# Optimization experiments

Hardware: AMD Instinct MI355X
Metric: run time of the kernel (lower is better)

## Reference

```python
import jax, jax.numpy as jnp
import numpy as np

B, N, E, R = 2, 4096, 1024, 128   # batch, seq_len, embed_dim, expand_ratio (head_dim)
H = E // R                        # num heads (scalar decay per head)
EPS = 1e-5                        # torch LayerNorm default eps


def _silu(x):
    return x * jax.nn.sigmoid(x)


def setup_inputs() -> dict:
    key = jax.random.key(0)
    ks = jax.random.split(key, 12)
    std = 0.02

    def w(k, shape):
        return jax.random.normal(k, shape, jnp.float32) * std

    return {
        "x": jax.random.normal(ks[0], (B, N, E), jnp.float32),
        # log of lower bound of the decay gate; must be negative so exp() in (0,1)
        "log_lower_bound": -jax.random.uniform(ks[1], (H,), jnp.float32, minval=0.1, maxval=3.0),
        "Wq": w(ks[2], (E, E)),
        "Wk": w(ks[3], (E, E)),
        "Wv": w(ks[4], (E, E)),
        "Wf": w(ks[5], (H, E)),      # f_proj: embed_dim -> embed_dim // expand_ratio
        "Wb1": w(ks[6], (R, E)),     # bet_proj low-rank
        "Wb2": w(ks[7], (E, R)),
        "Wg1": w(ks[8], (R, E)),     # output_gate low-rank
        "Wg2": w(ks[9], (E, R)),
        "gamma": jnp.ones((E,), jnp.float32),  # LayerNorm weight (bias=False)
        "Wo": w(ks[10], (E, E)),
    }


def _simple_gla(q, k, v, g):
    """Gated linear attention recurrence (fla simple_gla semantics).
    q,k,v: [B,H,N,R]; g: [B,H,N] (log decay per head per step).
    S_t = exp(g_t) * S_{t-1} + k_t v_t^T ;  o_t = (q_t * d^-0.5) @ S_t
    """
    scale = q.shape[-1] ** -0.5
    qT = jnp.moveaxis(q, 2, 0)  # [N,B,H,R]
    kT = jnp.moveaxis(k, 2, 0)
    vT = jnp.moveaxis(v, 2, 0)
    gT = jnp.moveaxis(g, 2, 0)  # [N,B,H]

    S0 = jnp.zeros((q.shape[0], q.shape[1], q.shape[-1], v.shape[-1]), q.dtype)

    def step(S, inp):
        qt, kt, vt, gt = inp
        S = S * jnp.exp(gt)[..., None, None] + kt[..., :, None] * vt[..., None, :]
        o = jnp.einsum('bhk,bhkv->bhv', qt * scale, S)
        return S, o

    _, o = jax.lax.scan(step, S0, (qT, kT, vT, gT))
    return jnp.moveaxis(o, 0, 2)  # [B,H,N,R]


def reference(x, log_lower_bound, Wq, Wk, Wv, Wf, Wb1, Wb2, Wg1, Wg2, gamma, Wo):
    # projections + activations
    q = _silu(x @ Wq.T)
    k = _silu(x @ Wk.T)
    v = x @ Wv.T
    f = x @ Wf.T                      # [B,N,H] scalar decay logits per head

    # householder q-transform with dense-memory beta (normalized reflection vector)
    beta = _silu((x @ Wb1.T) @ Wb2.T)  # [B,N,E]
    bn = beta * jax.lax.rsqrt(jnp.sum(beta * beta, -1, keepdims=True) + 1e-12)
    q = q - 2.0 * jnp.sum(q * bn, -1, keepdims=True) * bn

    def split_heads(t):  # [B,N,E] -> [B,H,N,R]
        return jnp.moveaxis(t.reshape(B, N, H, R), 2, 1)

    qh, kh, vh = split_heads(q), split_heads(k), split_heads(v)

    # log-space decay gate with lower bound
    lb = jnp.exp(log_lower_bound)                      # [H] in (0,1)
    fg = lb + (1.0 - lb) * jax.nn.sigmoid(f)           # [B,N,H]
    log_f = jnp.transpose(jnp.log(fg), (0, 2, 1))      # [B,H,N]

    o = _simple_gla(qh, kh, vh, log_f)                 # [B,H,N,R]
    o = jnp.moveaxis(o, 1, 2).reshape(B, N, E)

    # output gate
    gate = jax.nn.sigmoid((x @ Wg1.T) @ Wg2.T)
    o = o * gate

    # LayerNorm (weight only, bias=False)
    mu = jnp.mean(o, -1, keepdims=True)
    var = jnp.mean((o - mu) ** 2, -1, keepdims=True)
    o = (o - mu) * jax.lax.rsqrt(var + EPS) * gamma

    return o @ Wo.T
```

## Files before the change

kernel.cpp:

```cpp
#include <hip/hip_runtime.h>
#include <hip/hip_bf16.h>

using u16 = unsigned short;
typedef __attribute__((ext_vector_type(8))) short bf16x8;
typedef __attribute__((ext_vector_type(4))) float f32x4;
typedef __attribute__((ext_vector_type(8))) u16 u16x8;
typedef __attribute__((ext_vector_type(4))) u16 u16x4;

#define B_ 2
#define N_ 4096
#define E_ 1024
#define R_ 128
#define H_ 8
#define M_ 8192
#define CHUNK_ 128
#define NC_ 32
#define BH_ 16

__device__ __forceinline__ float b2f(u16 u) { return __uint_as_float(((unsigned)u) << 16); }
__device__ __forceinline__ u16 f2b(float f) {
  unsigned u = __float_as_uint(f);
  return (u16)((u + 0x7fffu + ((u >> 16) & 1u)) >> 16);
}
__device__ __forceinline__ float sigm(float x) {
  return __builtin_amdgcn_rcpf(1.0f + __expf(-x));
}

#define GLDS(g, l) __builtin_amdgcn_global_load_lds( \
    (const __attribute__((address_space(1))) unsigned int*)(g), \
    (__attribute__((address_space(3))) unsigned int*)(l), 16, 0, 0)

struct CvtArgs {
  const float* src[10];
  u16* dst[11];
};

__global__ void __launch_bounds__(256) cvt_all(CvtArgs a) {
  int idx = blockIdx.x * 256 + threadIdx.x;
  const int SZ[11] = {2097152, 262144, 262144, 262144, 2048,
                      32768, 32768, 32768, 32768, 262144, 30720};
  int off = idx, seg = 0;
#pragma unroll
  for (int i = 0; i < 10; i++) {
    if (seg == i && off >= SZ[i]) { off -= SZ[i]; seg = i + 1; }
  }
  u16x4 z = (u16x4){0, 0, 0, 0};
  if (seg == 10) { ((u16x4*)a.dst[10])[off] = z; return; }
  float4 v = ((const float4*)a.src[seg])[off];
  u16x4 r;
  r[0] = f2b(v.x); r[1] = f2b(v.y); r[2] = f2b(v.z); r[3] = f2b(v.w);
  if (seg == 6) {
    int n = off >> 5, c = off & 31;
    u16x4* W2 = (u16x4*)a.dst[6];
    W2[n * 64 + c] = r; W2[n * 64 + 32 + c] = z;
  } else if (seg == 8) {
    int n = off >> 5, c = off & 31;
    u16x4* W2 = (u16x4*)a.dst[8];
    W2[(1024 + n) * 64 + 32 + c] = r; W2[(1024 + n) * 64 + c] = z;
  } else {
    ((u16x4*)a.dst[seg])[off] = r;
  }
}

template<bool SWAP>
__device__ __forceinline__ void mfma_panel(f32x4 (&acc)[4][4], const u16* A, const u16* Bm,
                                           int wr, int wc, int l15, int q8) {
  bf16x8 af[4], bf[4];
#pragma unroll
  for (int mi = 0; mi < 4; mi++) af[mi] = *(const bf16x8*)&A[(wr * 64 + mi * 16 + l15) * 32 + q8];
#pragma unroll
  for (int ni = 0; ni < 4; ni++) bf[ni] = *(const bf16x8*)&Bm[(wc * 64 + ni * 16 + l15) * 32 + q8];
#pragma unroll
  for (int mi = 0; mi < 4; mi++)
#pragma unroll
    for (int ni = 0; ni < 4; ni++)
      acc[mi][ni] = SWAP
        ? __builtin_amdgcn_mfma_f32_16x16x32_bf16(bf[ni], af[mi], acc[mi][ni], 0, 0, 0)
        : __builtin_amdgcn_mfma_f32_16x16x32_bf16(af[mi], bf[ni], acc[mi][ni], 0, 0, 0);
}

template<bool SWAP, int K>
__device__ __forceinline__ void gemm_loop(const u16* __restrict__ X, const u16* __restrict__ W,
                                          int m0, int n0,
                                          u16* As, u16* Bs, f32x4 (&acc)[4][4], int tid) {
  const int wave = tid >> 6, lane = tid & 63;
  const int wr = wave >> 1, wc = wave & 1, l15 = lane & 15, q8 = (lane >> 4) * 8;
  const u16* Ap = X + (size_t)(m0 + wave * 32 + (lane >> 2)) * K + (lane & 3) * 8;
  const u16* Bp = W + (size_t)(n0 + wave * 32 + (lane >> 2)) * K + (lane & 3) * 8;
  u16* A0 = As + wave * 1024;
  u16* B0 = Bs + wave * 1024;
#pragma unroll
  for (int k0 = 0; k0 < K; k0 += 64) {
    GLDS(Ap + k0,                    A0);
    GLDS(Ap + 16 * (size_t)K + k0,   A0 + 512);
    GLDS(Ap + k0 + 32,               A0 + 4096);
    GLDS(Ap + 16 * (size_t)K + k0 + 32, A0 + 4608);
    GLDS(Bp + k0,                    B0);
    GLDS(Bp + 16 * (size_t)K + k0,   B0 + 512);
    GLDS(Bp + k0 + 32,               B0 + 4096);
    GLDS(Bp + 16 * (size_t)K + k0 + 32, B0 + 4608);
    __syncthreads();
    mfma_panel<SWAP>(acc, As, Bs, wr, wc, l15, q8);
    mfma_panel<SWAP>(acc, As + 4096, Bs + 4096, wr, wc, l15, q8);
    __syncthreads();
  }
}

__global__ void __launch_bounds__(256) mega_gemm(const u16* __restrict__ X, const u16* __restrict__ Wcat,
                                                 const float* __restrict__ llb,
                                                 u16* __restrict__ Qb, u16* __restrict__ Kb,
                                                 u16* __restrict__ KT, u16* __restrict__ VT,
                                                 u16* __restrict__ T1, float* __restrict__ LOGF) {
  __shared__ u16 sh[17408];
  u16* As = sh;
  u16* Bs = sh + 8192;
  u16* Ts = sh;
  const int tid = threadIdx.x;
  const int m0 = blockIdx.y * 128;
  const int ny = blockIdx.x, n0 = ny * 128;
  const int wave = tid >> 6, lane = tid & 63;
  const int wr = wave >> 1, wc = wave & 1, l15 = lane & 15, q4 = (lane >> 4) * 4;
  f32x4 acc[4][4];
#pragma unroll
  for (int i = 0; i < 4; i++)
#pragma unroll
    for (int j = 0; j < 4; j++) acc[i][j] = (f32x4){0.f, 0.f, 0.f, 0.f};

  if (ny >= 16 && ny < 24) {
    gemm_loop<false, 1024>(X, Wcat, m0, n0, As, Bs, acc, tid);
#pragma unroll
    for (int mi = 0; mi < 4; mi++) {
#pragma unroll
      for (int ni = 0; ni < 4; ni++) {
        int col = n0 - 2048 + wc * 64 + ni * 16 + l15;
        int rbase = m0 + wr * 64 + mi * 16 + q4;
        int head = col >> 7, rl = col & 127;
        int bb = rbase >> 12, nseq = rbase & (N_ - 1);
        u16x4 pk;
#pragma unroll
        for (int r = 0; r < 4; r++) pk[r] = f2b(acc[mi][ni][r]);
        *(u16x4*)&VT[((size_t)(bb * H_ + head) * R_ + rl) * N_ + nseq] = pk;
      }
    }
    return;
  }

  gemm_loop<true, 1024>(X, Wcat, m0, n0, As, Bs, acc, tid);

  if (ny == 26) {
    if (wc == 0 && (lane >> 4) < 2) {
#pragma unroll
      for (int mi = 0; mi < 4; mi++) {
        int mcol = m0 + wr * 64 + mi * 16 + l15;
        int bb = mcol >> 12, nseq = mcol & (N_ - 1);
#pragma unroll
        for (int r = 0; r < 4; r++) {
          int h = q4 + r;
          float lb = __expf(llb[h]);
          LOGF[(size_t)(bb * H_ + h) * N_ + nseq] =
              __logf(lb + (1.f - lb) * sigm(acc[mi][0][r]));
        }
      }
    }
    return;
  }

#pragma unroll
  for (int mi = 0; mi < 4; mi++) {
#pragma unroll
    for (int ni = 0; ni < 4; ni++) {
      int nb = n0 + wc * 64 + ni * 16 + q4;
      int mcol = m0 + wr * 64 + mi * 16 + l15;
      u16x4 pk;
#pragma unroll
      for (int r = 0; r < 4; r++) {
        float v = acc[mi][ni][r];
        if (ny < 16) v = v * sigm(v);
        pk[r] = f2b(v);
      }
      if (ny < 8) {
        *(u16x4*)&Qb[(size_t)mcol * E_ + nb] = pk;
      } else if (ny < 16) {
        *(u16x4*)&Kb[(size_t)mcol * E_ + nb - 1024] = pk;
        int nl = nb - n0;
        int ml = mcol - m0;
#pragma unroll
        for (int r = 0; r < 4; r++) Ts[(nl + r) * 136 + ml] = pk[r];
      } else {
        *(u16x4*)&T1[(size_t)mcol * 256 + nb - 3072] = pk;
      }
    }
  }

  if (ny >= 8 && ny < 16) {
    __syncthreads();
    int head = (n0 - 1024) >> 7;
    int bb = m0 >> 12, nloc = m0 & (N_ - 1);
    size_t base = ((size_t)(bb * H_ + head) * R_) * N_ + nloc;
#pragma unroll
    for (int p = 0; p < 8; p++) {
      int nl = p * 16 + (tid >> 4);
      int m8 = (tid & 15) * 8;
      u16x8 v = *(const u16x8*)&Ts[nl * 136 + m8];
      *(u16x8*)&KT[base + (size_t)nl * N_ + m8] = v;
    }
  }
}

__global__ void __launch_bounds__(256) bg_gemm(const u16* __restrict__ T1, const u16* __restrict__ W2,
                                               u16* __restrict__ BETA, u16* __restrict__ GATE) {
  __shared__ u16 As[8192];
  __shared__ u16 Bs[8192];
  const int tid = threadIdx.x;
  const int m0 = blockIdx.x * 128;
  const int n0 = blockIdx.y * 128;
  f32x4 acc[4][4];
#pragma unroll
  for (int i = 0; i < 4; i++)
#pragma unroll
    for (int j = 0; j < 4; j++) acc[i][j] = (f32x4){0.f, 0.f, 0.f, 0.f};
  gemm_loop<true, 256>(T1, W2, m0, n0, As, Bs, acc, tid);
  const int wave = tid >> 6, lane = tid & 63;
  const int wr = wave >> 1, wc = wave & 1, l15 = lane & 15, q4 = (lane >> 4) * 4;
#pragma unroll
  for (int mi = 0; mi < 4; mi++) {
#pragma unroll
    for (int ni = 0; ni < 4; ni++) {
      int nb = n0 + wc * 64 + ni * 16 + q4;
      int mcol = m0 + wr * 64 + mi * 16 + l15;
      u16x4 pk;
      if (nb < 1024) {
#pragma unroll
        for (int r = 0; r < 4; r++) {
          float v = acc[mi][ni][r];
          pk[r] = f2b(v * sigm(v));
        }
        *(u16x4*)&BETA[(size_t)mcol * E_ + nb] = pk;
      } else {
#pragma unroll
        for (int r = 0; r < 4; r++) pk[r] = f2b(sigm(acc[mi][ni][r]));
        *(u16x4*)&GATE[(size_t)mcol * E_ + nb - 1024] = pk;
      }
    }
  }
}

__global__ void __launch_bounds__(256) out_gemm(const u16* __restrict__ X, const u16* __restrict__ W,
                                                float* __restrict__ C) {
  __shared__ u16 As[8192];
  __shared__ u16 Bs[8192];
  const int tid = threadIdx.x;
  const int m0 = blockIdx.x * 128;
  const int n0 = blockIdx.y * 128;
  f32x4 acc[4][4];
#pragma unroll
  for (int i = 0; i < 4; i++)
#pragma unroll
    for (int j = 0; j < 4; j++) acc[i][j] = (f32x4){0.f, 0.f, 0.f, 0.f};
  gemm_loop<true, 1024>(X, W, m0, n0, As, Bs, acc, tid);
  const int wave = tid >> 6, lane = tid & 63;
  const int wr = wave >> 1, wc = wave & 1, l15 = lane & 15, q4 = (lane >> 4) * 4;
#pragma unroll
  for (int mi = 0; mi < 4; mi++) {
#pragma unroll
    for (int ni = 0; ni < 4; ni++) {
      int nb = n0 + wc * 64 + ni * 16 + q4;
      int mcol = m0 + wr * 64 + mi * 16 + l15;
      *(f32x4*)&C[(size_t)mcol * E_ + nb] = acc[mi][ni];
    }
  }
}

__global__ void __launch_bounds__(256) householder(u16* __restrict__ Q, const u16* __restrict__ BETA) {
  int row = blockIdx.x;
  int tid = threadIdx.x;
  u16* q = Q + (size_t)row * E_;
  const u16* bt = BETA + (size_t)row * E_;
  u16x4 q4 = *(const u16x4*)(q + tid * 4);
  u16x4 b4 = *(const u16x4*)(bt + tid * 4);
  float qv[4], bv[4];
#pragma unroll
  for (int i = 0; i < 4; i++) { qv[i] = b2f(q4[i]); bv[i] = b2f(b4[i]); }
  float ss = bv[0]*bv[0] + bv[1]*bv[1] + bv[2]*bv[2] + bv[3]*bv[3];
  float qd = qv[0]*bv[0] + qv[1]*bv[1] + qv[2]*bv[2] + qv[3]*bv[3];
  __shared__ float red[8];
#pragma unroll
  for (int m = 1; m < 64; m <<= 1) { ss += __shfl_xor(ss, m); qd += __shfl_xor(qd, m); }
  int wid = tid >> 6;
  if ((tid & 63) == 0) { red[wid] = ss; red[4 + wid] = qd; }
  __syncthreads();
  ss = red[0] + red[1] + red[2] + red[3];
  qd = red[4] + red[5] + red[6] + red[7];
  float coef = 2.f * qd / (ss + 1e-12f);
  const float scale = 0.08838834764831845f;
  u16x4 o4;
#pragma unroll
  for (int i = 0; i < 4; i++) o4[i] = f2b((qv[i] - coef * bv[i]) * scale);
  *(u16x4*)(q + tid * 4) = o4;
}

__device__ __forceinline__ void scan_chunk(const float* __restrict__ lf, float* cum, int tid) {
  if (tid < 64) {
    float a = lf[tid], b = lf[tid + 64];
#pragma unroll
    for (int off = 1; off < 64; off <<= 1) {
      float t = __shfl_up(a, off);  if (tid >= off) a += t;
      float t2 = __shfl_up(b, off); if (tid >= off) b += t2;
    }
    b += __shfl(a, 63);
    cum[tid] = a; cum[tid + 64] = b;
  }
  __syncthreads();
}

__device__ __forceinline__ void stage32(u16* dst, const u16* src, size_t stride, int tid) {
  int r0 = tid >> 2, c8 = (tid & 3) * 8;
  *(u16x8*)&dst[(size_t)r0 * 40 + c8] = *(const u16x8*)&src[(size_t)r0 * stride + c8];
  int r1 = r0 + 64;
  *(u16x8*)&dst[(size_t)r1 * 40 + c8] = *(const u16x8*)&src[(size_t)r1 * stride + c8];
}

__device__ __forceinline__ void stage32_scaled(u16* dst, const u16* src, size_t stride,
                                               const float* w, int j0, int tid) {
  int c8 = (tid & 3) * 8;
  float wv[8];
#pragma unroll
  for (int i = 0; i < 8; i++) wv[i] = w[j0 + c8 + i];
#pragma unroll
  for (int rr = 0; rr < 128; rr += 64) {
    int r = rr + (tid >> 2);
    u16x8 raw = *(const u16x8*)&src[(size_t)r * stride + c8];
    u16x8 o;
#pragma unroll
    for (int i = 0; i < 8; i++) o[i] = f2b(b2f(raw[i]) * wv[i]);
    *(u16x8*)&dst[(size_t)r * 40 + c8] = o;
  }
}

template<bool SWAP>
__device__ __forceinline__ void mfma16(f32x4 (&acc)[4][4], const u16* A, const u16* Bm,
                                       int wr, int wc, int l15, int q8) {
  bf16x8 af[4], bf[4];
#pragma unroll
  for (int mi = 0; mi < 4; mi++) af[mi] = *(const bf16x8*)&A[(wr * 64 + mi * 16 + l15) * 40 + q8];
#pragma unroll
  for (int ni = 0; ni < 4; ni++) bf[ni] = *(const bf16x8*)&Bm[(wc * 64 + ni * 16 + l15) * 40 + q8];
#pragma unroll
  for (int mi = 0; mi < 4; mi++)
#pragma unroll
    for (int ni = 0; ni < 4; ni++)
      acc[mi][ni] = SWAP
        ? __builtin_amdgcn_mfma_f32_16x16x32_bf16(bf[ni], af[mi], acc[mi][ni], 0, 0, 0)
        : __builtin_amdgcn_mfma_f32_16x16x32_bf16(af[mi], bf[ni], acc[mi][ni], 0, 0, 0);
}

__global__ void __launch_bounds__(256) gla_phaseA(const u16* __restrict__ KT, const u16* __restrict__ VT,
                                                  const float* __restrict__ LOGF,
                                                  u16* __restrict__ U, float* __restrict__ DC) {
  const int blk = blockIdx.x;
  const int bh = blk >> 5, c = blk & 31;
  const int tid = threadIdx.x;
  const int wave = tid >> 6, lane = tid & 63;
  const int wr = wave >> 1, wc = wave & 1, l15 = lane & 15, q8 = (lane >> 4) * 8;
  __shared__ u16 SA[128 * 40];
  __shared__ u16 SB[128 * 40];
  __shared__ float cum[CHUNK_];
  __shared__ float wd[CHUNK_];
  scan_chunk(LOGF + (size_t)bh * N_ + c * CHUNK_, cum, tid);
  if (tid < 128) wd[tid] = __expf(cum[127] - cum[tid]);
  __syncthreads();
  const u16* vbase = VT + ((size_t)bh * R_) * N_ + (size_t)c * CHUNK_;
  const u16* kbase = KT + ((size_t)bh * R_) * N_ + (size_t)c * CHUNK_;
  f32x4 acc[4][4];
#pragma unroll
  for (int i = 0; i < 4; i++)
#pragma unroll
    for (int j = 0; j < 4; j++) acc[i][j] = (f32x4){0.f, 0.f, 0.f, 0.f};
  for (int j0 = 0; j0 < CHUNK_; j0 += 32) {
    __syncthreads();
    stage32(SA, vbase + j0, N_, tid);
    stage32_scaled(SB, kbase + j0, N_, wd, j0, tid);
    __syncthreads();
    mfma16<true>(acc, SA, SB, wr, wc, l15, q8);
  }
  u16* Up = U + (size_t)blk * (R_ * R_);
  const int q4 = (lane >> 4) * 4;
#pragma unroll
  for (int mi = 0; mi < 4; mi++) {
#pragma unroll
    for (int ni = 0; ni < 4; ni++) {
      int v = wr * 64 + mi * 16 + l15;
      int kb = wc * 64 + ni * 16 + q4;
      u16x4 pk;
#pragma unroll
      for (int r = 0; r < 4; r++) pk[r] = f2b(acc[mi][ni][r]);
      *(u16x4*)&Up[(size_t)v * R_ + kb] = pk;
    }
  }
  if (tid == 0) DC[blk] = __expf(cum[127]);
}

__global__ void __launch_bounds__(256) gla_phaseB(const u16* __restrict__ U, const float* __restrict__ DC,
                                                  u16* __restrict__ SSb) {
  int idx = blockIdx.x * 256 + threadIdx.x;
  int bh = idx >> 14;
  int e = idx & 16383;
  float s = 0.f;
  for (int c = 0; c < NC_; c++) {
    size_t off = ((size_t)bh * NC_ + c) * 16384 + e;
    SSb[off] = f2b(s);
    s = DC[bh * NC_ + c] * s + b2f(U[off]);
  }
}

__global__ void __launch_bounds__(256) gla_phaseC(const u16* __restrict__ Qb, const u16* __restrict__ Kb,
                                                  const u16* __restrict__ VT, const u16* __restrict__ SSb,
                                                  const float* __restrict__ LOGF, u16* __restrict__ Ob) {
  const int blk = blockIdx.x;
  const int bh = blk >> 5, c = blk & 31;
  const int b = bh >> 3, h = bh & 7;
  const int tid = threadIdx.x;
  const int wave = tid >> 6, lane = tid & 63;
  const int wr = wave >> 1, wc = wave & 1, l15 = lane & 15;
  const int q4i = (lane >> 4) * 4, q8 = (lane >> 4) * 8;
  __shared__ u16 SA[128 * 40];
  __shared__ u16 SB[128 * 40];
  __shared__ u16 Ps[128 * 136];
  __shared__ float cum[CHUNK_];
  __shared__ float cumE[CHUNK_];
  scan_chunk(LOGF + (size_t)bh * N_ + c * CHUNK_, cum, tid);
  if (tid < 128) cumE[tid] = __expf(cum[tid]);
  __syncthreads();
  const size_t rowbase = ((size_t)(b * N_ + c * CHUNK_)) * E_ + (size_t)h * R_;
  const u16* vtbase = VT + ((size_t)bh * R_) * N_ + (size_t)c * CHUNK_;
  const u16* ssbase = SSb + (size_t)blk * (R_ * R_);

  f32x4 acc[4][4];
#pragma unroll
  for (int i = 0; i < 4; i++)
#pragma unroll
    for (int j = 0; j < 4; j++) acc[i][j] = (f32x4){0.f, 0.f, 0.f, 0.f};

  for (int r0 = 0; r0 < R_; r0 += 32) {
    __syncthreads();
    stage32(SA, Kb + rowbase + r0, E_, tid);
    stage32(SB, Qb + rowbase + r0, E_, tid);
    __syncthreads();
    mfma16<false>(acc, SA, SB, wr, wc, l15, q8);
  }
#pragma unroll
  for (int mi = 0; mi < 4; mi++) {
#pragma unroll
    for (int ni = 0; ni < 4; ni++) {
      int jb = wr * 64 + mi * 16 + q4i;
      int i = wc * 64 + ni * 16 + l15;
      float ci = cum[i];
      float4 cj = *(const float4*)&cum[jb];
      u16x4 pk;
      float cjv[4] = {cj.x, cj.y, cj.z, cj.w};
#pragma unroll
      for (int r = 0; r < 4; r++) {
        int j = jb + r;
        float w = (j <= i) ? __expf(ci - cjv[r]) : 0.f;
        pk[r] = f2b(acc[mi][ni][r] * w);
      }
      *(u16x4*)&Ps[i * 136 + jb] = pk;
    }
  }
#pragma unroll
  for (int i = 0; i < 4; i++)
#pragma unroll
    for (int j = 0; j < 4; j++) acc[i][j] = (f32x4){0.f, 0.f, 0.f, 0.f};
  for (int k0 = 0; k0 < R_; k0 += 32) {
    __syncthreads();
    stage32(SA, Qb + rowbase + k0, E_, tid);
    stage32(SB, ssbase + k0, R_, tid);
    __syncthreads();
    mfma16<true>(acc, SA, SB, wr, wc, l15, q8);
  }
#pragma unroll
  for (int mi = 0; mi < 4; mi++) {
    float ei = cumE[wr * 64 + mi * 16 + l15];
#pragma unroll
    for (int ni = 0; ni < 4; ni++)
#pragma unroll
      for (int r = 0; r < 4; r++) acc[mi][ni][r] *= ei;
  }
  for (int j0 = 0; j0 < CHUNK_; j0 += 32) {
    __syncthreads();
    stage32(SB, vtbase + j0, N_, tid);
    __syncthreads();
    if (wr == 1 || j0 < 64) {
      bf16x8 af[4], bf[4];
#pragma unroll
      for (int mi = 0; mi < 4; mi++)
        af[mi] = *(const bf16x8*)&Ps[(wr * 64 + mi * 16 + l15) * 136 + j0 + q8];
#pragma unroll
      for (int ni = 0; ni < 4; ni++)
        bf[ni] = *(const bf16x8*)&SB[(wc * 64 + ni * 16 + l15) * 40 + q8];
#pragma unroll
      for (int mi = 0; mi < 4; mi++)
#pragma unroll
        for (int ni = 0; ni < 4; ni++)
          acc[mi][ni] = __builtin_amdgcn_mfma_f32_16x16x32_bf16(bf[ni], af[mi], acc[mi][ni], 0, 0, 0);
    }
  }
#pragma unroll
  for (int mi = 0; mi < 4; mi++) {
#pragma unroll
    for (int ni = 0; ni < 4; ni++) {
      int i = wr * 64 + mi * 16 + l15;
      int vb = wc * 64 + ni * 16 + q4i;
      u16x4 pk;
#pragma unroll
      for (int r = 0; r < 4; r++) pk[r] = f2b(acc[mi][ni][r]);
      *(u16x4*)&Ob[rowbase + (size_t)i * E_ + vb] = pk;
    }
  }
}

__global__ void __launch_bounds__(256) gate_ln(const u16* __restrict__ O, const u16* __restrict__ G,
                                               const float* __restrict__ gamma, u16* __restrict__ OLN) {
  int row = blockIdx.x, tid = threadIdx.x;
  u16x4 o4 = *(const u16x4*)(O + (size_t)row * E_ + tid * 4);
  u16x4 g4 = *(const u16x4*)(G + (size_t)row * E_ + tid * 4);
  float x0 = b2f(o4[0]) * b2f(g4[0]), x1 = b2f(o4[1]) * b2f(g4[1]);
  float x2 = b2f(o4[2]) * b2f(g4[2]), x3 = b2f(o4[3]) * b2f(g4[3]);
  float s = x0 + x1 + x2 + x3;
  float sq = x0 * x0 + x1 * x1 + x2 * x2 + x3 * x3;
  __shared__ float red[8];
#pragma unroll
  for (int m = 1; m < 64; m <<= 1) { s += __shfl_xor(s, m); sq += __shfl_xor(sq, m); }
  int wid = tid >> 6;
  if ((tid & 63) == 0) { red[wid] = s; red[4 + wid] = sq; }
  __syncthreads();
  s = red[0] + red[1] + red[2] + red[3];
  sq = red[4] + red[5] + red[6] + red[7];
  float mu = s * (1.f / 1024.f);
  float var = sq * (1.f / 1024.f) - mu * mu;
  float rs = rsqrtf(var + 1e-5f);
  int e = tid * 4;
  u16x4 r4;
  r4[0] = f2b((x0 - mu) * rs * gamma[e + 0]);
  r4[1] = f2b((x1 - mu) * rs * gamma[e + 1]);
  r4[2] = f2b((x2 - mu) * rs * gamma[e + 2]);
  r4[3] = f2b((x3 - mu) * rs * gamma[e + 3]);
  *(u16x4*)(OLN + (size_t)row * E_ + e) = r4;
}

extern "C" void kernel_launch(void* const* d_in, const int* in_sizes, int n_in,
                              void* d_out, int out_size, void* d_ws, size_t ws_size,
                              hipStream_t stream) {
  (void)in_sizes; (void)n_in; (void)out_size; (void)ws_size;
  const float* x   = (const float*)d_in[0];
  const float* llb = (const float*)d_in[1];
  const float* Wq  = (const float*)d_in[2];
  const float* Wk  = (const float*)d_in[3];
  const float* Wv  = (const float*)d_in[4];
  const float* Wf  = (const float*)d_in[5];
  const float* Wb1 = (const float*)d_in[6];
  const float* Wb2 = (const float*)d_in[7];
  const float* Wg1 = (const float*)d_in[8];
  const float* Wg2 = (const float*)d_in[9];
  const float* gm  = (const float*)d_in[10];
  const float* Wo  = (const float*)d_in[11];
  float* out = (float*)d_out;

  char* ws = (char*)d_ws;
  const size_t SZB = (size_t)M_ * E_ * 2;
  u16*   Qb    = (u16*)(ws + 0 * SZB);
  u16*   Kb    = (u16*)(ws + 1 * SZB);
  u16*   KT    = (u16*)(ws + 2 * SZB);
  u16*   VT    = (u16*)(ws + 3 * SZB);
  u16*   BETAb = (u16*)(ws + 4 * SZB);
  u16*   GATEb = (u16*)(ws + 5 * SZB);
  u16*   SSb   = (u16*)(ws + 6 * SZB);
  u16*   XB    = (u16*)(ws + 7 * SZB);
  u16*   U     = (u16*)(ws + 8 * SZB);
  char*  tail  = ws + 8 * SZB + (size_t)BH_ * NC_ * R_ * R_ * 2;
  u16*   Wcat  = (u16*)tail;
  u16*   Wcat2 = Wcat + (size_t)3456 * 1024;
  u16*   WOb   = Wcat2 + (size_t)2048 * 256;
  u16*   T1    = WOb + (size_t)E_ * E_;
  float* LOGF  = (float*)(T1 + (size_t)M_ * 256);
  float* DC    = LOGF + (size_t)BH_ * N_;
  u16*   Ob    = BETAb;
  u16*   OLN   = Qb;

  CvtArgs ca;
  ca.src[0] = x;   ca.dst[0]  = XB;
  ca.src[1] = Wq;  ca.dst[1]  = Wcat;
  ca.src[2] = Wk;  ca.dst[2]  = Wcat + (size_t)1024 * 1024;
  ca.src[3] = Wv;  ca.dst[3]  = Wcat + (size_t)2048 * 1024;
  ca.src[4] = Wf;  ca.dst[4]  = Wcat + (size_t)3328 * 1024;
  ca.src[5] = Wb1; ca.dst[5]  = Wcat + (size_t)3072 * 1024;
  ca.src[6] = Wb2; ca.dst[6]  = Wcat2;
  ca.src[7] = Wg1; ca.dst[7]  = Wcat + (size_t)3200 * 1024;
  ca.src[8] = Wg2; ca.dst[8]  = Wcat2;
  ca.src[9] = Wo;  ca.dst[9]  = WOb;
  ca.dst[10] = Wcat + (size_t)3336 * 1024;

  dim3 blk(256);
  cvt_all<<<dim3(12928), blk, 0, stream>>>(ca);
  mega_gemm<<<dim3(27, 64), blk, 0, stream>>>(XB, Wcat, llb, Qb, Kb, KT, VT, T1, LOGF);
  bg_gemm<<<dim3(64, 16), blk, 0, stream>>>(T1, Wcat2, BETAb, GATEb);
  householder<<<dim3(M_), blk, 0, stream>>>(Qb, BETAb);
  gla_phaseA<<<dim3(BH_ * NC_), blk, 0, stream>>>(KT, VT, LOGF, U, DC);
  gla_phaseB<<<dim3(BH_ * 16384 / 256), blk, 0, stream>>>(U, DC, SSb);
  gla_phaseC<<<dim3(BH_ * NC_), blk, 0, stream>>>(Qb, Kb, VT, SSb, LOGF, Ob);
  gate_ln<<<dim3(M_), blk, 0, stream>>>(Ob, GATEb, gm, OLN);
  out_gemm<<<dim3(64, 8), blk, 0, stream>>>(OLN, WOb, out);
}
```

Before: 310.4 us.

## Replace fused projection GEMM with 256x256-tile double-buffered pipelined kernel

```diff
diff --git a/kernel.cpp b/kernel.cpp
--- a/kernel.cpp
+++ b/kernel.cpp
@@ -106,58 +106,173 @@
   }
 }
 
-__global__ void __launch_bounds__(256) mega_gemm(const u16* __restrict__ X, const u16* __restrict__ Wcat,
-                                                 const float* __restrict__ llb,
-                                                 u16* __restrict__ Qb, u16* __restrict__ Kb,
-                                                 u16* __restrict__ KT, u16* __restrict__ VT,
-                                                 u16* __restrict__ T1, float* __restrict__ LOGF) {
-  __shared__ u16 sh[17408];
-  u16* As = sh;
-  u16* Bs = sh + 8192;
-  u16* Ts = sh;
+__global__ void __launch_bounds__(512, 2) mega_gemm256(
+    const u16* __restrict__ X, const u16* __restrict__ Wcat,
+    const float* __restrict__ llb,
+    u16* __restrict__ Qb, u16* __restrict__ Kb,
+    u16* __restrict__ KT, u16* __restrict__ VT,
+    u16* __restrict__ T1, float* __restrict__ LOGF) {
+  __shared__ u16 sh[65536];
   const int tid = threadIdx.x;
-  const int m0 = blockIdx.y * 128;
-  const int ny = blockIdx.x, n0 = ny * 128;
-  const int wave = tid >> 6, lane = tid & 63;
-  const int wr = wave >> 1, wc = wave & 1, l15 = lane & 15, q4 = (lane >> 4) * 4;
-  f32x4 acc[4][4];
-#pragma unroll
-  for (int i = 0; i < 4; i++)
+  const int w = tid >> 6, lane = tid & 63;
+  const int wr = w >> 2, wc = w & 3;
+  const int l15 = lane & 15, g = lane >> 4;
+  const int l7 = l15 & 7;
+
+  int flat = blockIdx.x;
+  int swz = (flat & 7) * 56 + (flat >> 3);
+  const int nt = swz % 14, mt = swz / 14;
+  const int m0 = mt * 256, n0 = nt * 256;
+
+  u16* const A0 = sh;
+  u16* const B0 = sh + 16384;
+  u16* const A1 = sh + 32768;
+  u16* const B1 = sh + 49152;
+  u16* const bufA[2] = {A0, A1};
+  u16* const bufB[2] = {B0, B1};
+
+  const int lrow = lane >> 3;
+  const int lcol = ((lane & 7) ^ lrow) * 8;
+  const int rbA[4] = {0, 128, 64, 192};
+  const int rbB[4] = {0, 64, 128, 192};
+  const u16* pA[4];
+  const u16* pB[4];
+#pragma unroll
+  for (int c = 0; c < 4; c++) {
+    pA[c] = X + (size_t)(m0 + rbA[c] + w * 8 + lrow) * 1024 + lcol;
+    int rho = rbB[c] + w * 8 + lrow;
+    int nh = rho >> 7, rr = rho & 127;
+    int nsrc = nh * 32 + ((rr >> 5) << 6) + (rr & 31);
+    pB[c] = Wcat + (size_t)(n0 + nsrc) * 1024 + lcol;
+  }
+
+  const int arow = (wr * 128 + l15) * 128;
+  const int brow = (wc * 32 + l15) * 128;
+  const int sA0 = (g ^ l7) << 4;
+  const int sA1 = sA0 ^ 64;
+
+  f32x4 acc[8][4];
+#pragma unroll
+  for (int i = 0; i < 8; i++)
 #pragma unroll
     for (int j = 0; j < 4; j++) acc[i][j] = (f32x4){0.f, 0.f, 0.f, 0.f};
 
-  if (ny >= 16 && ny < 24) {
-    gemm_loop<false, 1024>(X, Wcat, m0, n0, As, Bs, acc, tid);
-#pragma unroll
-    for (int mi = 0; mi < 4; mi++) {
+#define SA(T, c) GLDS(pA[c] + (size_t)(T) * 64, \
+    (u16*)((char*)bufA[(T) & 1] + rbA[c] * 128 + w * 1024))
+#define SB(T, c) GLDS(pB[c] + (size_t)(T) * 64, \
+    (u16*)((char*)bufB[(T) & 1] + rbB[c] * 128 + w * 1024))
+
+#define PHASE(Ab, Bb, MH, NH, STAGES, WAITOP)                                   \
+  {                                                                             \
+    bf16x8 af[4][2], bf[2][2];                                                  \
+    const char* Abase = (const char*)(Ab) + arow + (MH) * 8192;                 \
+    const char* Bbase = (const char*)(Bb) + brow + (NH) * 16384;                \
+    _Pragma("unroll") for (int mi2 = 0; mi2 < 4; mi2++) {                       \
+      af[mi2][0] = *(const bf16x8*)(Abase + mi2 * 2048 + sA0);                  \
+      af[mi2][1] = *(const bf16x8*)(Abase + mi2 * 2048 + sA1);                  \
+    }                                                                           \
+    _Pragma("unroll") for (int ni2 = 0; ni2 < 2; ni2++) {                       \
+      bf[ni2][0] = *(const bf16x8*)(Bbase + ni2 * 2048 + sA0);                  \
+      bf[ni2][1] = *(const bf16x8*)(Bbase + ni2 * 2048 + sA1);                  \
+    }                                                                           \
+    STAGES;                                                                     \
+    __builtin_amdgcn_sched_barrier(0);                                          \
+    __builtin_amdgcn_s_barrier();                                               \
+    asm volatile("s_waitcnt lgkmcnt(0)" ::: "memory");                          \
+    __builtin_amdgcn_sched_barrier(0);                                          \
+    __builtin_amdgcn_s_setprio(1);                                              \
+    _Pragma("unroll") for (int mi2 = 0; mi2 < 4; mi2++)                         \
+      _Pragma("unroll") for (int ni2 = 0; ni2 < 2; ni2++) {                     \
+        acc[(MH)*4+mi2][(NH)*2+ni2] = __builtin_amdgcn_mfma_f32_16x16x32_bf16(  \
+            bf[ni2][0], af[mi2][0], acc[(MH)*4+mi2][(NH)*2+ni2], 0, 0, 0);      \
+        acc[(MH)*4+mi2][(NH)*2+ni2] = __builtin_amdgcn_mfma_f32_16x16x32_bf16(  \
+            bf[ni2][1], af[mi2][1], acc[(MH)*4+mi2][(NH)*2+ni2], 0, 0, 0);      \
+      }                                                                         \
+    __builtin_amdgcn_s_setprio(0);                                              \
+    WAITOP;                                                                     \
+    __builtin_amdgcn_sched_barrier(0);                                          \
+    __builtin_amdgcn_s_barrier();                                               \
+    __builtin_amdgcn_sched_barrier(0);                                          \
+  }
+
+#define NOOP ((void)0)
+#define ITER(i, LAST)                                                           \
+  PHASE(A0, B0, 0, 0, { SA(2*(i)+1, 2); SA(2*(i)+1, 3); }, NOOP);               \
+  PHASE(A0, B0, 0, 1, { SB(2*(i)+1, 2); SB(2*(i)+1, 3); }, NOOP);               \
+  PHASE(A0, B0, 1, 0, { if (!(LAST)) { SA(2*(i)+2, 0); SA(2*(i)+2, 1); } }, NOOP); \
+  PHASE(A0, B0, 1, 1, { if (!(LAST)) { SB(2*(i)+2, 0); SB(2*(i)+2, 1); } },     \
+        { if (LAST) { asm volatile("s_waitcnt vmcnt(0)" ::: "memory"); }        \
+          else      { asm volatile("s_waitcnt vmcnt(4)" ::: "memory"); } });    \
+  PHASE(A1, B1, 0, 0, { if (!(LAST)) { SA(2*(i)+2, 2); SA(2*(i)+2, 3); } }, NOOP); \
+  PHASE(A1, B1, 0, 1, { if (!(LAST)) { SB(2*(i)+2, 2); SB(2*(i)+2, 3); } }, NOOP); \
+  PHASE(A1, B1, 1, 0, { if (!(LAST)) { SA(2*(i)+3, 0); SA(2*(i)+3, 1); } }, NOOP); \
+  PHASE(A1, B1, 1, 1, { if (!(LAST)) { SB(2*(i)+3, 0); SB(2*(i)+3, 1); } },     \
+        { if (!(LAST)) { asm volatile("s_waitcnt vmcnt(4)" ::: "memory"); } });
+
+  SA(0, 0); SA(0, 1); SB(0, 0); SB(0, 1);
+  SA(0, 2); SA(0, 3); SB(0, 2); SB(0, 3);
+  SA(1, 0); SA(1, 1); SB(1, 0); SB(1, 1);
+  asm volatile("s_waitcnt vmcnt(4)" ::: "memory");
+  __builtin_amdgcn_sched_barrier(0);
+  __builtin_amdgcn_s_barrier();
+  __builtin_amdgcn_sched_barrier(0);
+
+#pragma unroll 1
+  for (int i = 0; i < 7; ++i) {
+    ITER(i, 0)
+  }
+  ITER(7, 1)
+
+#undef ITER
+#undef PHASE
+#undef SA
+#undef SB
+#undef NOOP
+
+  const int q4 = g * 4;
+  const int b = m0 >> 12;
+  const int nseq0 = m0 & (N_ - 1);
+
+  if (nt < 4) {
+#pragma unroll
+    for (int mi = 0; mi < 8; mi++) {
+      size_t mrow = (size_t)(m0 + wr * 128 + (mi >> 2) * 64 + (mi & 3) * 16 + l15);
 #pragma unroll
       for (int ni = 0; ni < 4; ni++) {
-        int col = n0 - 2048 + wc * 64 + ni * 16 + l15;
-        int rbase = m0 + wr * 64 + mi * 16 + q4;
-        int head = col >> 7, rl = col & 127;
-        int bb = rbase >> 12, nseq = rbase & (N_ - 1);
+        int nc = n0 + wc * 64 + (ni >> 1) * 32 + (ni & 1) * 16 + q4;
         u16x4 pk;
 #pragma unroll
+        for (int r = 0; r < 4; r++) { float v = acc[mi][ni][r]; pk[r] = f2b(v * sigm(v)); }
+        *(u16x4*)&Qb[mrow * E_ + nc] = pk;
+      }
+    }
+    return;
+  }
+  if (nt == 12) {
+#pragma unroll
+    for (int mi = 0; mi < 8; mi++) {
+      size_t mrow = (size_t)(m0 + wr * 128 + (mi >> 2) * 64 + (mi & 3) * 16 + l15);
+#pragma unroll
+      for (int ni = 0; ni < 4; ni++) {
+        int nc = n0 - 3072 + wc * 64 + (ni >> 1) * 32 + (ni & 1) * 16 + q4;
+        u16x4 pk;
+#pragma unroll
         for (int r = 0; r < 4; r++) pk[r] = f2b(acc[mi][ni][r]);
-        *(u16x4*)&VT[((size_t)(bb * H_ + head) * R_ + rl) * N_ + nseq] = pk;
+        *(u16x4*)&T1[mrow * 256 + nc] = pk;
       }
     }
     return;
   }
-
-  gemm_loop<true, 1024>(X, Wcat, m0, n0, As, Bs, acc, tid);
-
-  if (ny == 26) {
-    if (wc == 0 && (lane >> 4) < 2) {
-#pragma unroll
-      for (int mi = 0; mi < 4; mi++) {
-        int mcol = m0 + wr * 64 + mi * 16 + l15;
-        int bb = mcol >> 12, nseq = mcol & (N_ - 1);
+  if (nt == 13) {
+    if (wc == 0 && g < 2) {
+#pragma unroll
+      for (int mi = 0; mi < 8; mi++) {
+        int nseq = nseq0 + wr * 128 + (mi >> 2) * 64 + (mi & 3) * 16 + l15;
 #pragma unroll
         for (int r = 0; r < 4; r++) {
           int h = q4 + r;
           float lb = __expf(llb[h]);
-          LOGF[(size_t)(bb * H_ + h) * N_ + nseq] =
+          LOGF[(size_t)(b * H_ + h) * N_ + nseq] =
               __logf(lb + (1.f - lb) * sigm(acc[mi][0][r]));
         }
       }
@@ -165,45 +280,56 @@
     return;
   }
 
-#pragma unroll
-  for (int mi = 0; mi < 4; mi++) {
-#pragma unroll
-    for (int ni = 0; ni < 4; ni++) {
-      int nb = n0 + wc * 64 + ni * 16 + q4;
-      int mcol = m0 + wr * 64 + mi * 16 + l15;
-      u16x4 pk;
-#pragma unroll
-      for (int r = 0; r < 4; r++) {
-        float v = acc[mi][ni][r];
-        if (ny < 16) v = v * sigm(v);
-        pk[r] = f2b(v);
+  const bool isK = nt < 8;
+  if (isK) {
+#pragma unroll
+    for (int mi = 0; mi < 8; mi++) {
+      size_t mrow = (size_t)(m0 + wr * 128 + (mi >> 2) * 64 + (mi & 3) * 16 + l15);
+#pragma unroll
+      for (int ni = 0; ni < 4; ni++) {
+        int nc = n0 - 1024 + wc * 64 + (ni >> 1) * 32 + (ni & 1) * 16 + q4;
+        u16x4 pk;
+#pragma unroll
+        for (int r = 0; r < 4; r++) { float v = acc[mi][ni][r]; pk[r] = f2b(v * sigm(v)); }
+        *(u16x4*)&Kb[mrow * E_ + nc] = pk;
       }
-      if (ny < 8) {
-        *(u16x4*)&Qb[(size_t)mcol * E_ + nb] = pk;
-      } else if (ny < 16) {
-        *(u16x4*)&Kb[(size_t)mcol * E_ + nb - 1024] = pk;
-        int nl = nb - n0;
-        int ml = mcol - m0;
-#pragma unroll
-        for (int r = 0; r < 4; r++) Ts[(nl + r) * 136 + ml] = pk[r];
-      } else {
-        *(u16x4*)&T1[(size_t)mcol * 256 + nb - 3072] = pk;
+    }
+  }
+  u16* Ts = sh;
+  u16* DST = isK ? KT : VT;
+  const int head0 = (n0 - (isK ? 1024 : 2048)) >> 7;
+  __syncthreads();
+#pragma unroll
+  for (int pass = 0; pass < 2; pass++) {
+    if (wr == pass) {
+#pragma unroll
+      for (int mi = 0; mi < 8; mi++) {
+        int ml = (mi >> 2) * 64 + (mi & 3) * 16 + l15;
+#pragma unroll
+        for (int ni = 0; ni < 4; ni++) {
+          int nl = wc * 64 + (ni >> 1) * 32 + (ni & 1) * 16 + q4;
+#pragma unroll
+          for (int r = 0; r < 4; r++) {
+            float v = acc[mi][ni][r];
+            if (isK) v = v * sigm(v);
+            Ts[(nl + r) * 136 + ml] = f2b(v);
+          }
+        }
       }
     }
-  }
-
-  if (ny >= 8 && ny < 16) {
-    __syncthreads();
-    int head = (n0 - 1024) >> 7;
-    int bb = m0 >> 12, nloc = m0 & (N_ - 1);
-    size_t base = ((size_t)(bb * H_ + head) * R_) * N_ + nloc;
-#pragma unroll
-    for (int p = 0; p < 8; p++) {
-      int nl = p * 16 + (tid >> 4);
-      int m8 = (tid & 15) * 8;
-      u16x8 v = *(const u16x8*)&Ts[nl * 136 + m8];
-      *(u16x8*)&KT[base + (size_t)nl * N_ + m8] = v;
-    }
+    __syncthreads();
+    {
+      int row = tid >> 1;
+      int colb = (tid & 1) * 64;
+      size_t drow = ((size_t)(b * H_ + head0 + (row >> 7)) * R_ + (row & 127)) * (size_t)N_;
+      size_t seqb = (size_t)nseq0 + pass * 128 + colb;
+#pragma unroll
+      for (int j = 0; j < 8; j++) {
+        u16x8 v = *(const u16x8*)&Ts[row * 136 + colb + j * 8];
+        *(u16x8*)&DST[drow + seqb + j * 8] = v;
+      }
+    }
+    if (pass == 0) __syncthreads();
   }
 }
 
@@ -602,7 +728,7 @@
 
   dim3 blk(256);
   cvt_all<<<dim3(12928), blk, 0, stream>>>(ca);
-  mega_gemm<<<dim3(27, 64), blk, 0, stream>>>(XB, Wcat, llb, Qb, Kb, KT, VT, T1, LOGF);
+  mega_gemm256<<<dim3(448), dim3(512), 0, stream>>>(XB, Wcat, llb, Qb, Kb, KT, VT, T1, LOGF);
   bg_gemm<<<dim3(64, 16), blk, 0, stream>>>(T1, Wcat2, BETAb, GATEb);
   householder<<<dim3(M_), blk, 0, stream>>>(Qb, BETAb);
   gla_phaseA<<<dim3(BH_ * NC_), blk, 0, stream>>>(KT, VT, LOGF, U, DC);
```

Measured after the change: 318.4 us. +2.6%, slower.

## Double-buffer projection GEMM LDS staging with swizzled layout and setprio

Applied to the files above, without the earlier changes.

```diff
diff --git a/kernel.cpp b/kernel.cpp
--- a/kernel.cpp
+++ b/kernel.cpp
@@ -106,14 +106,64 @@
   }
 }
 
-__global__ void __launch_bounds__(256) mega_gemm(const u16* __restrict__ X, const u16* __restrict__ Wcat,
-                                                 const float* __restrict__ llb,
-                                                 u16* __restrict__ Qb, u16* __restrict__ Kb,
-                                                 u16* __restrict__ KT, u16* __restrict__ VT,
-                                                 u16* __restrict__ T1, float* __restrict__ LOGF) {
+template<bool SWAP>
+__device__ __forceinline__ void gemm128_dbuf(const u16* __restrict__ X, const u16* __restrict__ W,
+                                             int m0, int n0, u16* sh, f32x4 (&acc)[4][4], int tid) {
+  const int w = tid >> 6, lane = tid & 63;
+  const int wr = w >> 1, wc = w & 1;
+  const int l15 = lane & 15, g = lane >> 4;
+  const int lrow = tid >> 2;
+  const int scol = (tid & 3) ^ ((lrow ^ (lrow >> 2)) & 3);
+  const u16* pA0 = X + (size_t)(m0 + lrow) * 1024 + scol * 8;
+  const u16* pA1 = X + (size_t)(m0 + 64 + lrow) * 1024 + scol * 8;
+  const u16* pB0 = W + (size_t)(n0 + lrow) * 1024 + scol * 8;
+  const u16* pB1 = W + (size_t)(n0 + 64 + lrow) * 1024 + scol * 8;
+  const int sw = (g ^ (l15 & 3) ^ ((l15 >> 2) & 3)) << 4;
+  const int abase = (wr * 64 + l15) * 64 + sw;
+  const int bbase = (wc * 64 + l15) * 64 + sw;
+
+#define STG128(T, bi) do {                                                      \
+    char* Ad_ = (char*)sh + (bi) * 16384;                                       \
+    char* Bd_ = (char*)sh + 8192 + (bi) * 16384;                                \
+    GLDS(pA0 + (size_t)(T) * 32, Ad_ + w * 1024);                               \
+    GLDS(pA1 + (size_t)(T) * 32, Ad_ + 4096 + w * 1024);                        \
+    GLDS(pB0 + (size_t)(T) * 32, Bd_ + w * 1024);                               \
+    GLDS(pB1 + (size_t)(T) * 32, Bd_ + 4096 + w * 1024);                        \
+  } while (0)
+
+  STG128(0, 0);
+  __syncthreads();
+
+#pragma unroll 2
+  for (int t = 0; t < 32; ++t) {
+    if (t < 31) STG128(t + 1, (t + 1) & 1);
+    const char* Ab = (const char*)sh + (t & 1) * 16384;
+    const char* Bb = (const char*)sh + 8192 + (t & 1) * 16384;
+    bf16x8 af[4], bf[4];
+#pragma unroll
+    for (int mi = 0; mi < 4; mi++) af[mi] = *(const bf16x8*)(Ab + abase + mi * 1024);
+#pragma unroll
+    for (int ni = 0; ni < 4; ni++) bf[ni] = *(const bf16x8*)(Bb + bbase + ni * 1024);
+    __builtin_amdgcn_s_setprio(1);
+#pragma unroll
+    for (int mi = 0; mi < 4; mi++)
+#pragma unroll
+      for (int ni = 0; ni < 4; ni++)
+        acc[mi][ni] = SWAP
+          ? __builtin_amdgcn_mfma_f32_16x16x32_bf16(bf[ni], af[mi], acc[mi][ni], 0, 0, 0)
+          : __builtin_amdgcn_mfma_f32_16x16x32_bf16(af[mi], bf[ni], acc[mi][ni], 0, 0, 0);
+    __builtin_amdgcn_s_setprio(0);
+    __syncthreads();
+  }
+#undef STG128
+}
+
+__global__ void __launch_bounds__(256, 4) mega_gemm(const u16* __restrict__ X, const u16* __restrict__ Wcat,
+                                                    const float* __restrict__ llb,
+                                                    u16* __restrict__ Qb, u16* __restrict__ Kb,
+                                                    u16* __restrict__ KT, u16* __restrict__ VT,
+                                                    u16* __restrict__ T1, float* __restrict__ LOGF) {
   __shared__ u16 sh[17408];
-  u16* As = sh;
-  u16* Bs = sh + 8192;
   u16* Ts = sh;
   const int tid = threadIdx.x;
   const int m0 = blockIdx.y * 128;
@@ -127,7 +177,7 @@
     for (int j = 0; j < 4; j++) acc[i][j] = (f32x4){0.f, 0.f, 0.f, 0.f};
 
   if (ny >= 16 && ny < 24) {
-    gemm_loop<false, 1024>(X, Wcat, m0, n0, As, Bs, acc, tid);
+    gemm128_dbuf<false>(X, Wcat, m0, n0, sh, acc, tid);
 #pragma unroll
     for (int mi = 0; mi < 4; mi++) {
 #pragma unroll
@@ -145,7 +195,7 @@
     return;
   }
 
-  gemm_loop<true, 1024>(X, Wcat, m0, n0, As, Bs, acc, tid);
+  gemm128_dbuf<true>(X, Wcat, m0, n0, sh, acc, tid);
 
   if (ny == 26) {
     if (wc == 0 && (lane >> 4) < 2) {
```

Result: no change. 310.1 us (-0.1%).
